# Kernel tuning notes

Measured on AMD Instinct MI355X. Metric: run time of the kernel, lower is better.

## Reference

```python
import jax, jax.numpy as jnp
import numpy as np

B, C, IN_H, IN_W = 32, 16, 64, 64
OUT_H, OUT_W, K, STRIDE = 60, 60, 5, 1


def setup_inputs() -> dict:
    key = jax.random.key(0)
    k1, k2 = jax.random.split(key)
    # spike-like inputs in [0,1)
    in_spikes = jax.random.uniform(k1, (B, C, IN_H, IN_W), dtype=jnp.float32)
    # unshared locally-connected weights: (outH, outW, C_in, K, K, C_out)
    weights = jax.random.normal(k2, (OUT_H, OUT_W, C, K, K, C), dtype=jnp.float32) * (1.0 / (K * K))
    return {"in_spikes": in_spikes, "weights": weights}


def _extract_patches(x, out_h, out_w, k, stride):
    # x: (B, C, H, W) -> patches: (B, C, K, K, out_h, out_w)
    # static K*K loop over kernel offsets (not a data-dim loop)
    rows = []
    for di in range(k):
        cols = []
        for dj in range(k):
            cols.append(x[:, :, di:di + out_h * stride:stride, dj:dj + out_w * stride:stride])
        rows.append(jnp.stack(cols, axis=2))  # (B, C, K, out_h, out_w)
    return jnp.stack(rows, axis=2)  # (B, C, K, K, out_h, out_w)


def reference(in_spikes, weights):
    out_h, out_w, _, k, _, _ = weights.shape
    patches = _extract_patches(in_spikes, out_h, out_w, k, STRIDE)
    # output[b, k_out, i, j] = sum_{c,u,v} patches[b,c,u,v,i,j] * weights[i,j,c,u,v,k_out]
    out = jnp.einsum('bcuvij,ijcuvk->bkij', patches, weights)
    return out
```

## Files before the change

kernel.cpp:

```cpp
#include <hip/hip_runtime.h>
#include <hip/hip_bf16.h>


#define OUT_HW 60
#define IN_HW  64
#define CIN    16
#define COUT   16
#define KS     5
#define MTOT   400
#define NB     32
#define NPOS   3600
#define BK     512
#define CHW    65536
#define XSTR   424

typedef __attribute__((ext_vector_type(8))) short bf16x8;
typedef __attribute__((ext_vector_type(4))) float f32x4;

static __device__ __forceinline__ unsigned pk2(float a, float b) {
    union { __hip_bfloat162 h; unsigned u; } cv;
    cv.h = __float22bfloat162_rn(make_float2(a, b));
    return cv.u;
}

__global__ __launch_bounds__(256)
void transpose_x(const float* __restrict__ x, float* __restrict__ xt) {
    __shared__ float tile[32][65];
    const int n0 = blockIdx.x * 64;
    const int t  = threadIdx.x;
    const int tx = t & 63, ty = t >> 6;
    for (int bb = ty; bb < 32; bb += 4)
        tile[bb][tx] = x[(size_t)bb * CHW + n0 + tx];
    __syncthreads();
    const int b = t & 31;
    for (int nn = t >> 5; nn < 64; nn += 8)
        xt[(size_t)(n0 + nn) * 32 + b] = tile[b][nn];
}

template<int USEXT, int PACKED>
__global__ __launch_bounds__(256)
void lc_mfma(const float* __restrict__ xsrc, const float* __restrict__ w,
             float* __restrict__ dst) {
    __shared__ ushort sW[COUT * XSTR] __attribute__((aligned(16)));
    __shared__ ushort sX[NB * XSTR]  __attribute__((aligned(16)));
    __shared__ int    sLUT[MTOT]     __attribute__((aligned(16)));
    __shared__ float  sRed[4][NB * 17];

    const int bid = blockIdx.x;
    const int i = bid / OUT_HW, j = bid - i * OUT_HW;
    const int t = threadIdx.x;
    const float* wpos = w + (size_t)bid * (MTOT * COUT);

    for (int m = t; m < MTOT; m += 256) {
        const int c = m / 25, r = m - c * 25, u = r / 5, v = r - u * 5;
        const int n = c * (IN_HW * IN_HW) + u * IN_HW + v;
        sLUT[m] = USEXT ? n * NB : n;
    }
    sW[(t >> 4) * XSTR + 400 + (t & 15)] = 0;
    for (int e = t; e < 512; e += 256)
        sX[(e >> 4) * XSTR + 400 + (e & 15)] = 0;
    __syncthreads();

    {
        const int k = t & 15;
        for (int mg = t >> 4; mg < 50; mg += 16) {
            const float* s = wpos + mg * 128 + k;
            float f[8];
#pragma unroll
            for (int jj = 0; jj < 8; ++jj) f[jj] = s[jj * 16];
            union { bf16x8 v; unsigned u[4]; } p;
#pragma unroll
            for (int jj = 0; jj < 4; ++jj) p.u[jj] = pk2(f[2 * jj], f[2 * jj + 1]);
            *(bf16x8*)&sW[k * XSTR + mg * 8] = p.v;
        }
    }
    {
        const int b = t & 31;
        const int xoff = USEXT ? ((i * IN_HW + j) * NB + b)
                               : (b * CHW + i * IN_HW + j);
        for (int mg = t >> 5; mg < 50; mg += 8) {
            const int4 L0 = *(const int4*)&sLUT[mg * 8];
            const int4 L1 = *(const int4*)&sLUT[mg * 8 + 4];
            float f[8];
            f[0] = xsrc[L0.x + xoff]; f[1] = xsrc[L0.y + xoff];
            f[2] = xsrc[L0.z + xoff]; f[3] = xsrc[L0.w + xoff];
            f[4] = xsrc[L1.x + xoff]; f[5] = xsrc[L1.y + xoff];
            f[6] = xsrc[L1.z + xoff]; f[7] = xsrc[L1.w + xoff];
            union { bf16x8 v; unsigned u[4]; } p;
#pragma unroll
            for (int jj = 0; jj < 4; ++jj) p.u[jj] = pk2(f[2 * jj], f[2 * jj + 1]);
            *(bf16x8*)&sX[b * XSTR + mg * 8] = p.v;
        }
    }
    __syncthreads();

    const int lane = t & 63, wv = t >> 6;
    const int l15 = lane & 15, q = lane >> 4;
    f32x4 acc0 = {0.f, 0.f, 0.f, 0.f}, acc1 = {0.f, 0.f, 0.f, 0.f};
    const ushort* pB  = &sW[l15 * XSTR + q * 8];
    const ushort* pA0 = &sX[l15 * XSTR + q * 8];
    const ushort* pA1 = &sX[(l15 + 16) * XSTR + q * 8];
    for (int c = wv; c < 13; c += 4) {
        const bf16x8 bF = *(const bf16x8*)(pB  + c * 32);
        const bf16x8 a0 = *(const bf16x8*)(pA0 + c * 32);
        const bf16x8 a1 = *(const bf16x8*)(pA1 + c * 32);
        acc0 = __builtin_amdgcn_mfma_f32_16x16x32_bf16(a0, bF, acc0, 0, 0, 0);
        acc1 = __builtin_amdgcn_mfma_f32_16x16x32_bf16(a1, bF, acc1, 0, 0, 0);
    }

#pragma unroll
    for (int r = 0; r < 4; ++r) {
        sRed[wv][(q * 4 + r) * 17 + l15]      = acc0[r];
        sRed[wv][(q * 4 + r + 16) * 17 + l15] = acc1[r];
    }
    __syncthreads();
#pragma unroll
    for (int h = 0; h < 2; ++h) {
        const int o = t + h * 256;
        const int idx = (o >> 4) * 17 + (o & 15);
        const float sv = sRed[0][idx] + sRed[1][idx] + sRed[2][idx] + sRed[3][idx];
        if (PACKED) dst[(size_t)bid * BK + o] = sv;
        else        dst[(size_t)o * NPOS + bid] = sv;
    }
}

__global__ __launch_bounds__(256)
void transpose_out(const float* __restrict__ src, float* __restrict__ out) {
    __shared__ float tile[64][65];
    const int o0 = blockIdx.x * 64;
    const int k0 = blockIdx.y * 64;
    const int t  = threadIdx.x;
    const int tx = t & 63, ty = t >> 6;
    for (int r = ty; r < 64; r += 4) {
        const int oij = o0 + r;
        if (oij < NPOS) tile[r][tx] = src[(size_t)oij * BK + k0 + tx];
    }
    __syncthreads();
    for (int r = ty; r < 64; r += 4) {
        const int oij = o0 + tx;
        if (oij < NPOS) out[(size_t)(k0 + r) * NPOS + oij] = tile[tx][r];
    }
}

extern "C" void kernel_launch(void* const* d_in, const int* in_sizes, int n_in,
                              void* d_out, int out_size, void* d_ws, size_t ws_size,
                              hipStream_t stream) {
    const float* x = (const float*)d_in[0];
    const float* w = (const float*)d_in[1];
    float* out = (float*)d_out;
    float* xt  = (float*)d_ws;

    const size_t xtBytes  = (size_t)CHW * NB * 4;
    const size_t outBytes = (size_t)NPOS * BK * 4;
    if (ws_size >= xtBytes + outBytes) {
        float* wsOut = xt + (size_t)CHW * NB;
        transpose_x<<<CHW / 64, 256, 0, stream>>>(x, xt);
        lc_mfma<1, 1><<<NPOS, 256, 0, stream>>>(xt, w, wsOut);
        transpose_out<<<dim3((NPOS + 63) / 64, BK / 64), 256, 0, stream>>>(wsOut, out);
    } else if (ws_size >= xtBytes) {
        transpose_x<<<CHW / 64, 256, 0, stream>>>(x, xt);
        lc_mfma<1, 0><<<NPOS, 256, 0, stream>>>(xt, w, out);
    } else {
        lc_mfma<0, 0><<<NPOS, 256, 0, stream>>>(x, w, out);
    }
}
```

Before: 172.8 us.

## Store input as channel-last bf16 and feed MFMA fragments directly from global memory

Replaces the fp32 batch-major transpose with a bf16 channel-last copy of the input. MFMA A fragments are loaded straight from global memory as 8 contiguous channels, so the per-block LDS gather of input patches goes away. Weights are staged raw as fp32 in LDS with vectorised float4 loads and converted to bf16 per fragment. Blocks are remapped across positions for better cache locality, and a naive fallback kernel is added for small workspaces. The cost is uncoalesced per-lane global loads in the MFMA loop and repeated bf16 conversions.

```diff
diff --git a/kernel.cpp b/kernel.cpp
--- a/kernel.cpp
+++ b/kernel.cpp
@@ -6,13 +6,9 @@
 #define IN_HW  64
 #define CIN    16
 #define COUT   16
-#define KS     5
-#define MTOT   400
-#define NB     32
 #define NPOS   3600
 #define BK     512
-#define CHW    65536
-#define XSTR   424
+#define XC_ELE (32u * 64u * 64u * 16u)
 
 typedef __attribute__((ext_vector_type(8))) short bf16x8;
 typedef __attribute__((ext_vector_type(4))) float f32x4;
@@ -24,88 +20,81 @@
 }
 
 __global__ __launch_bounds__(256)
-void transpose_x(const float* __restrict__ x, float* __restrict__ xt) {
-    __shared__ float tile[32][65];
-    const int n0 = blockIdx.x * 64;
-    const int t  = threadIdx.x;
-    const int tx = t & 63, ty = t >> 6;
-    for (int bb = ty; bb < 32; bb += 4)
-        tile[bb][tx] = x[(size_t)bb * CHW + n0 + tx];
-    __syncthreads();
-    const int b = t & 31;
-    for (int nn = t >> 5; nn < 64; nn += 8)
-        xt[(size_t)(n0 + nn) * 32 + b] = tile[b][nn];
+void make_xc(const float* __restrict__ x, ushort* __restrict__ xc) {
+    const int bh = blockIdx.x;
+    const int b = bh >> 6, h = bh & 63;
+    const int t = threadIdx.x;
+    const int cq = t & 3, wc = t >> 2;
+    const float* src = x + ((size_t)(b * CIN) * IN_HW + h) * IN_HW + wc;
+    float f[4];
+#pragma unroll
+    for (int e = 0; e < 4; ++e)
+        f[e] = src[(size_t)(cq * 4 + e) * (IN_HW * IN_HW)];
+    union { ushort4 v; unsigned u[2]; } o;
+    o.u[0] = pk2(f[0], f[1]);
+    o.u[1] = pk2(f[2], f[3]);
+    *(ushort4*)&xc[((size_t)bh * IN_HW + wc) * CIN + cq * 4] = o.v;
 }
 
-template<int USEXT, int PACKED>
-__global__ __launch_bounds__(256)
-void lc_mfma(const float* __restrict__ xsrc, const float* __restrict__ w,
-             float* __restrict__ dst) {
-    __shared__ ushort sW[COUT * XSTR] __attribute__((aligned(16)));
-    __shared__ ushort sX[NB * XSTR]  __attribute__((aligned(16)));
-    __shared__ int    sLUT[MTOT]     __attribute__((aligned(16)));
-    __shared__ float  sRed[4][NB * 17];
+template<int PACKED>
+__global__ __launch_bounds__(256, 4)
+void lc_pos(const ushort* __restrict__ xc, const float* __restrict__ w,
+            float* __restrict__ dst) {
+    __shared__ float sWraw[400 * 20];
+    __shared__ float sRed[4][32 * 17];
 
     const int bid = blockIdx.x;
-    const int i = bid / OUT_HW, j = bid - i * OUT_HW;
+    const int pos = (bid & 7) * 450 + (bid >> 3);
+    const int i = pos / OUT_HW, j = pos - i * OUT_HW;
     const int t = threadIdx.x;
-    const float* wpos = w + (size_t)bid * (MTOT * COUT);
-
-    for (int m = t; m < MTOT; m += 256) {
-        const int c = m / 25, r = m - c * 25, u = r / 5, v = r - u * 5;
-        const int n = c * (IN_HW * IN_HW) + u * IN_HW + v;
-        sLUT[m] = USEXT ? n * NB : n;
-    }
-    sW[(t >> 4) * XSTR + 400 + (t & 15)] = 0;
-    for (int e = t; e < 512; e += 256)
-        sX[(e >> 4) * XSTR + 400 + (e & 15)] = 0;
-    __syncthreads();
 
     {
-        const int k = t & 15;
-        for (int mg = t >> 4; mg < 50; mg += 16) {
-            const float* s = wpos + mg * 128 + k;
-            float f[8];
+        const float4* wf4 = (const float4*)(w + (size_t)pos * 6400);
+        float4 vv[7];
 #pragma unroll
-            for (int jj = 0; jj < 8; ++jj) f[jj] = s[jj * 16];
-            union { bf16x8 v; unsigned u[4]; } p;
+        for (int it = 0; it < 7; ++it) {
+            const int f = t + (it << 8);
+            if (f < 1600) vv[it] = wf4[f];
+        }
 #pragma unroll
-            for (int jj = 0; jj < 4; ++jj) p.u[jj] = pk2(f[2 * jj], f[2 * jj + 1]);
-            *(bf16x8*)&sW[k * XSTR + mg * 8] = p.v;
-        }
-    }
-    {
-        const int b = t & 31;
-        const int xoff = USEXT ? ((i * IN_HW + j) * NB + b)
-                               : (b * CHW + i * IN_HW + j);
-        for (int mg = t >> 5; mg < 50; mg += 8) {
-            const int4 L0 = *(const int4*)&sLUT[mg * 8];
-            const int4 L1 = *(const int4*)&sLUT[mg * 8 + 4];
-            float f[8];
-            f[0] = xsrc[L0.x + xoff]; f[1] = xsrc[L0.y + xoff];
-            f[2] = xsrc[L0.z + xoff]; f[3] = xsrc[L0.w + xoff];
-            f[4] = xsrc[L1.x + xoff]; f[5] = xsrc[L1.y + xoff];
-            f[6] = xsrc[L1.z + xoff]; f[7] = xsrc[L1.w + xoff];
-            union { bf16x8 v; unsigned u[4]; } p;
-#pragma unroll
-            for (int jj = 0; jj < 4; ++jj) p.u[jj] = pk2(f[2 * jj], f[2 * jj + 1]);
-            *(bf16x8*)&sX[b * XSTR + mg * 8] = p.v;
+        for (int it = 0; it < 7; ++it) {
+            const int f = t + (it << 8);
+            if (f < 1600) {
+                const int m = f >> 2, k4 = (f & 3) << 2;
+                *(float4*)&sWraw[m * 20 + k4] = vv[it];
+            }
         }
     }
     __syncthreads();
 
     const int lane = t & 63, wv = t >> 6;
     const int l15 = lane & 15, q = lane >> 4;
+    const int qh = q >> 1, c0 = (q & 1) << 3;
     f32x4 acc0 = {0.f, 0.f, 0.f, 0.f}, acc1 = {0.f, 0.f, 0.f, 0.f};
-    const ushort* pB  = &sW[l15 * XSTR + q * 8];
-    const ushort* pA0 = &sX[l15 * XSTR + q * 8];
-    const ushort* pA1 = &sX[(l15 + 16) * XSTR + q * 8];
-    for (int c = wv; c < 13; c += 4) {
-        const bf16x8 bF = *(const bf16x8*)(pB  + c * 32);
-        const bf16x8 a0 = *(const bf16x8*)(pA0 + c * 32);
-        const bf16x8 a1 = *(const bf16x8*)(pA1 + c * 32);
-        acc0 = __builtin_amdgcn_mfma_f32_16x16x32_bf16(a0, bF, acc0, 0, 0, 0);
-        acc1 = __builtin_amdgcn_mfma_f32_16x16x32_bf16(a1, bF, acc1, 0, 0, 0);
+    const int base_hw = i * IN_HW + j;
+
+    for (int cc = wv; cc < 13; cc += 4) {
+        const int uvB = cc * 2 + qh;
+        const int okB = (uvB < 25);
+        float bfv[8];
+#pragma unroll
+        for (int jj = 0; jj < 8; ++jj) {
+            const int c = c0 + jj;
+            bfv[jj] = okB ? sWraw[(c * 25 + uvB) * 20 + l15] : 0.f;
+        }
+        union { bf16x8 v; unsigned u[4]; } pb;
+#pragma unroll
+        for (int jj = 0; jj < 4; ++jj) pb.u[jj] = pk2(bfv[2 * jj], bfv[2 * jj + 1]);
+
+        const int uvA = okB ? uvB : 24;
+        const int uA = (uvA * 13) >> 6;
+        const int vA = uvA - 5 * uA;
+        const size_t xoff = (size_t)l15 * (IN_HW * IN_HW * CIN)
+                          + (size_t)(base_hw + uA * IN_HW + vA) * CIN + c0;
+        const bf16x8 a0 = *(const bf16x8*)(xc + xoff);
+        const bf16x8 a1 = *(const bf16x8*)(xc + xoff + 16u * IN_HW * IN_HW * CIN);
+        acc0 = __builtin_amdgcn_mfma_f32_16x16x32_bf16(a0, pb.v, acc0, 0, 0, 0);
+        acc1 = __builtin_amdgcn_mfma_f32_16x16x32_bf16(a1, pb.v, acc1, 0, 0, 0);
     }
 
 #pragma unroll
@@ -119,8 +108,8 @@
         const int o = t + h * 256;
         const int idx = (o >> 4) * 17 + (o & 15);
         const float sv = sRed[0][idx] + sRed[1][idx] + sRed[2][idx] + sRed[3][idx];
-        if (PACKED) dst[(size_t)bid * BK + o] = sv;
-        else        dst[(size_t)o * NPOS + bid] = sv;
+        if (PACKED) dst[(size_t)pos * BK + o] = sv;
+        else        dst[(size_t)o * NPOS + pos] = sv;
     }
 }
 
@@ -142,25 +131,46 @@
     }
 }
 
+__global__ __launch_bounds__(256)
+void lc_naive(const float* __restrict__ x, const float* __restrict__ w,
+              float* __restrict__ out) {
+    const int gid = blockIdx.x * 256 + threadIdx.x;
+    if (gid >= 32 * COUT * NPOS) return;
+    const int j = gid % OUT_HW;
+    int rest = gid / OUT_HW;
+    const int i = rest % OUT_HW; rest /= OUT_HW;
+    const int k = rest % COUT;
+    const int b = rest / COUT;
+    const float* wp = w + (size_t)(i * OUT_HW + j) * 6400 + k;
+    float s = 0.f;
+    for (int c = 0; c < CIN; ++c)
+        for (int u = 0; u < 5; ++u)
+            for (int v = 0; v < 5; ++v)
+                s += x[((size_t)(b * CIN + c) * IN_HW + i + u) * IN_HW + j + v]
+                   * wp[((c * 5 + u) * 5 + v) * COUT];
+    out[gid] = s;
+}
+
 extern "C" void kernel_launch(void* const* d_in, const int* in_sizes, int n_in,
                               void* d_out, int out_size, void* d_ws, size_t ws_size,
                               hipStream_t stream) {
     const float* x = (const float*)d_in[0];
     const float* w = (const float*)d_in[1];
     float* out = (float*)d_out;
-    float* xt  = (float*)d_ws;
 
-    const size_t xtBytes  = (size_t)CHW * NB * 4;
+    const size_t xcBytes  = (size_t)XC_ELE * 2;
     const size_t outBytes = (size_t)NPOS * BK * 4;
-    if (ws_size >= xtBytes + outBytes) {
-        float* wsOut = xt + (size_t)CHW * NB;
-        transpose_x<<<CHW / 64, 256, 0, stream>>>(x, xt);
-        lc_mfma<1, 1><<<NPOS, 256, 0, stream>>>(xt, w, wsOut);
+    ushort* xc = (ushort*)d_ws;
+
+    if (ws_size >= xcBytes + outBytes) {
+        float* wsOut = (float*)((char*)d_ws + xcBytes);
+        make_xc<<<32 * IN_HW, 256, 0, stream>>>(x, xc);
+        lc_pos<1><<<NPOS, 256, 0, stream>>>(xc, w, wsOut);
         transpose_out<<<dim3((NPOS + 63) / 64, BK / 64), 256, 0, stream>>>(wsOut, out);
-    } else if (ws_size >= xtBytes) {
-        transpose_x<<<CHW / 64, 256, 0, stream>>>(x, xt);
-        lc_mfma<1, 0><<<NPOS, 256, 0, stream>>>(xt, w, out);
+    } else if (ws_size >= xcBytes) {
+        make_xc<<<32 * IN_HW, 256, 0, stream>>>(x, xc);
+        lc_pos<0><<<NPOS, 256, 0, stream>>>(xc, w, out);
     } else {
-        lc_mfma<0, 0><<<NPOS, 256, 0, stream>>>(x, w, out);
+        lc_naive<<<(32 * COUT * NPOS + 255) / 256, 256, 0, stream>>>(x, w, out);
     }
 }
```

After: 190.1 us. +10.0%, slower.
